# Performance work log

Measured on AMD Instinct MI355X. Metric: run time of the kernel, lower is better.

Reference implementation:

```python
import jax, jax.numpy as jnp
import numpy as np

B, L, D = 8, 2048, 512


def setup_inputs() -> dict:
    key = jax.random.key(0)
    ks = jax.random.split(key, 6)
    s = 0.02
    return {
        "q": jax.random.normal(ks[0], (B, L, D), jnp.float32),
        "k": jax.random.normal(ks[1], (B, L, D), jnp.float32),
        "v": jax.random.normal(ks[2], (B, L, D), jnp.float32),
        "Wq": jax.random.normal(ks[3], (D, D), jnp.float32) * s,
        "bq": jnp.zeros((D,), jnp.float32),
        "Wk": jax.random.normal(ks[4], (D, D), jnp.float32) * s,
        "bk": jnp.zeros((D,), jnp.float32),
        "Wv": jax.random.normal(ks[5], (D, D), jnp.float32) * s,
        "bv": jnp.zeros((D,), jnp.float32),
    }


def reference(q, k, v, Wq, bq, Wk, bk, Wv, bv):
    # Linear projections (torch Linear: x @ W.T + b)
    qp = jnp.einsum("bld,ed->ble", q, Wq) + bq
    kp = jnp.einsum("bld,ed->ble", k, Wk) + bk
    vp = jnp.einsum("bld,ed->ble", v, Wv) + bv
    # attn[b, i, j] = qp[b, i] . kp[b, j]   (no 1/sqrt(d) scaling in source)
    attn = jnp.einsum("bqd,bkd->bqk", qp, kp)
    # Faithful to torch.nn.Softmax(dim=1): normalize over the QUERY axis.
    attn = jax.nn.softmax(attn, axis=1)
    out = jnp.einsum("bqk,bkd->bqd", attn, vp)
    return out
```

## Files before the change

### kernel.cpp

```cpp
#include <hip/hip_runtime.h>
#include <math.h>


#define TKK 32

typedef __attribute__((ext_vector_type(8))) short bf16x8;
typedef __attribute__((ext_vector_type(4))) float floatx4;

typedef __attribute__((address_space(3))) short lds_short;
typedef const __attribute__((address_space(1))) short glob_short;

__device__ __forceinline__ short f2bf(float x) {
    unsigned u = __float_as_uint(x);
    u += 0x7fff + ((u >> 16) & 1);
    return (short)(u >> 16);
}
__device__ __forceinline__ float bf2f(short s) {
    return __uint_as_float(((unsigned)(unsigned short)s) << 16);
}
__device__ __forceinline__ float exp2_fast(float x) {
    float r;
    asm("v_exp_f32 %0, %1" : "=v"(r) : "v"(x));
    return r;
}

#define STAGE_SC(lane) ((((lane) & 3) ^ (((lane) >> 3) & 3)) * 8)
#define FRAG_FC(lane) (((((lane) >> 4) ^ (((lane) >> 1) & 3))) * 8)

__global__ __launch_bounds__(256) void prep(
    const float* __restrict__ q, const float* __restrict__ k,
    const float* __restrict__ v,
    const float* __restrict__ Wq, const float* __restrict__ Wk,
    const float* __restrict__ Wv,
    short* __restrict__ q_bf, short* __restrict__ k_bf, short* __restrict__ v_bf,
    short* __restrict__ Wq_bf, short* __restrict__ Wk_bf, short* __restrict__ Wv_bf,
    float* __restrict__ colsum)
{
    const int b = blockIdx.x;
    const float* in = nullptr;
    short* out = nullptr;
    long long i;
    if (b < 12288) {
        const int z = b >> 12;
        in  = (z == 0) ? q    : (z == 1) ? k    : v;
        out = (z == 0) ? q_bf : (z == 1) ? k_bf : v_bf;
        i = ((long long)(b & 4095) * 256 + threadIdx.x) * 8;
    } else if (b < 12672) {
        const int z = (b - 12288) >> 7;
        in  = (z == 0) ? Wq    : (z == 1) ? Wk    : Wv;
        out = (z == 0) ? Wq_bf : (z == 1) ? Wk_bf : Wv_bf;
        i = ((long long)((b - 12288) & 127) * 256 + threadIdx.x) * 8;
    } else {
        colsum[(b - 12672) * 256 + threadIdx.x] = 0.f;
        return;
    }
    float4 x = *(const float4*)(in + i);
    float4 y = *(const float4*)(in + i + 4);
    bf16x8 r;
    r[0] = f2bf(x.x); r[1] = f2bf(x.y); r[2] = f2bf(x.z); r[3] = f2bf(x.w);
    r[4] = f2bf(y.x); r[5] = f2bf(y.y); r[6] = f2bf(y.z); r[7] = f2bf(y.w);
    *(bf16x8*)(out + i) = r;
}

template<int TMp, int TNp, int WM, int WN, int HAS_BIAS, int OUT_BF16>
__device__ __forceinline__ void gemm_body(
    const short* __restrict__ A, const short* __restrict__ B,
    const float* __restrict__ bias, void* __restrict__ C,
    int N, int K, int m0, int n0, float escale)
{
    __shared__ short As[TMp * TKK];
    __shared__ short Bs[TNp * TKK];
    constexpr int MI = TMp / (16 * WM);
    constexpr int NJ = TNp / (16 * WN);
    constexpr int NWAVES = WM * WN;
    const int t    = threadIdx.x;
    const int wave = t >> 6;
    const int lane = t & 63;
    const int wm = (wave / WN) * (TMp / WM);
    const int wn = (wave % WN) * (TNp / WN);
    const int sr = lane >> 2;
    const int sc = STAGE_SC(lane);
    const int fc = FRAG_FC(lane);

    floatx4 acc[MI][NJ];
    #pragma unroll
    for (int i = 0; i < MI; ++i)
        #pragma unroll
        for (int j = 0; j < NJ; ++j)
            acc[i][j] = (floatx4){0.f, 0.f, 0.f, 0.f};

    for (int k0 = 0; k0 < K; k0 += TKK) {
        #pragma unroll
        for (int c = wave; c < TMp / 16; c += NWAVES)
            __builtin_amdgcn_global_load_lds(
                (glob_short*)(A + (long long)(m0 + c * 16 + sr) * K + k0 + sc),
                (lds_short*)(As + c * 512), 16, 0, 0);
        #pragma unroll
        for (int c = wave; c < TNp / 16; c += NWAVES)
            __builtin_amdgcn_global_load_lds(
                (glob_short*)(B + (long long)(n0 + c * 16 + sr) * K + k0 + sc),
                (lds_short*)(Bs + c * 512), 16, 0, 0);
        __syncthreads();
        bf16x8 af[MI], bfr[NJ];
        #pragma unroll
        for (int i = 0; i < MI; ++i)
            af[i] = *(const bf16x8*)&As[(wm + i * 16 + (lane & 15)) * TKK + fc];
        #pragma unroll
        for (int j = 0; j < NJ; ++j)
            bfr[j] = *(const bf16x8*)&Bs[(wn + j * 16 + (lane & 15)) * TKK + fc];
        #pragma unroll
        for (int i = 0; i < MI; ++i)
            #pragma unroll
            for (int j = 0; j < NJ; ++j)
                acc[i][j] = __builtin_amdgcn_mfma_f32_16x16x32_bf16(af[i], bfr[j], acc[i][j], 0, 0, 0);
        __syncthreads();
    }

    #pragma unroll
    for (int i = 0; i < MI; ++i) {
        const int rbase = m0 + wm + i * 16 + (lane >> 4) * 4;
        #pragma unroll
        for (int j = 0; j < NJ; ++j) {
            const int col = n0 + wn + j * 16 + (lane & 15);
            const float bb = HAS_BIAS ? bias[col] : 0.f;
            #pragma unroll
            for (int r = 0; r < 4; ++r) {
                const long long off = (long long)(rbase + r) * N + col;
                const float vvv = (acc[i][j][r] + bb) * escale;
                if (OUT_BF16) ((short*)C)[off] = f2bf(vvv);
                else          ((float*)C)[off] = vvv;
            }
        }
    }
}

__global__ __launch_bounds__(512) void proj_gemm(
    const short* __restrict__ x0, const short* __restrict__ x1, const short* __restrict__ x2,
    const short* __restrict__ w0, const short* __restrict__ w1, const short* __restrict__ w2,
    const float* __restrict__ b0, const float* __restrict__ b1, const float* __restrict__ b2,
    short* __restrict__ y0, short* __restrict__ y1, short* __restrict__ y2,
    int N, int K)
{
    const int z = blockIdx.z;
    const short* A    = (z == 0) ? x0 : (z == 1) ? x1 : x2;
    const short* B    = (z == 0) ? w0 : (z == 1) ? w1 : w2;
    const float* bias = (z == 0) ? b0 : (z == 1) ? b1 : b2;
    short*       C    = (z == 0) ? y0 : (z == 1) ? y1 : y2;
    const float esc   = (z == 0) ? 1.4426950408889634f : 1.0f;
    gemm_body<128, 128, 4, 2, 1, 1>(A, B, bias, C, N, K,
                                    blockIdx.x * 128, blockIdx.y * 128, esc);
}

__global__ __launch_bounds__(512) void pv_gemm(
    const short* __restrict__ Eg, const short* __restrict__ vpTg,
    float* __restrict__ outg, int N, int K,
    long long sA, long long sB, long long sC)
{
    __shared__ short As[2][128 * TKK];
    __shared__ short Bs[2][64 * TKK];
    const int bz = blockIdx.z;
    const short* A = Eg   + (long long)bz * sA;
    const short* B = vpTg + (long long)bz * sB;
    float*       C = outg + (long long)bz * sC;

    const int m0 = blockIdx.x * 128;
    const int n0 = blockIdx.y * 64;
    const int t    = threadIdx.x;
    const int wave = t >> 6;
    const int lane = t & 63;
    const int wm = (wave >> 1) * 32;
    const int wn = (wave & 1)  * 32;
    const int sr = lane >> 2;
    const int sc = STAGE_SC(lane);
    const int fc = FRAG_FC(lane);

    floatx4 acc[2][2];
    #pragma unroll
    for (int i = 0; i < 2; ++i)
        #pragma unroll
        for (int j = 0; j < 2; ++j)
            acc[i][j] = (floatx4){0.f, 0.f, 0.f, 0.f};

    for (int k0 = 0; k0 < K; k0 += 2 * TKK) {
        #pragma unroll
        for (int h = 0; h < 2; ++h) {
            const int kk = k0 + h * TKK;
            __builtin_amdgcn_global_load_lds(
                (glob_short*)(A + (long long)(m0 + wave * 16 + sr) * K + kk + sc),
                (lds_short*)(As[h] + wave * 512), 16, 0, 0);
            if (wave < 4)
                __builtin_amdgcn_global_load_lds(
                    (glob_short*)(B + (long long)(n0 + wave * 16 + sr) * K + kk + sc),
                    (lds_short*)(Bs[h] + wave * 512), 16, 0, 0);
        }
        __syncthreads();
        #pragma unroll
        for (int h = 0; h < 2; ++h) {
            bf16x8 af[2], bfr[2];
            #pragma unroll
            for (int i = 0; i < 2; ++i)
                af[i] = *(const bf16x8*)&As[h][(wm + i * 16 + (lane & 15)) * TKK + fc];
            #pragma unroll
            for (int j = 0; j < 2; ++j)
                bfr[j] = *(const bf16x8*)&Bs[h][(wn + j * 16 + (lane & 15)) * TKK + fc];
            #pragma unroll
            for (int i = 0; i < 2; ++i)
                #pragma unroll
                for (int j = 0; j < 2; ++j)
                    acc[i][j] = __builtin_amdgcn_mfma_f32_16x16x32_bf16(af[i], bfr[j], acc[i][j], 0, 0, 0);
        }
        __syncthreads();
    }

    #pragma unroll
    for (int i = 0; i < 2; ++i) {
        const int rbase = m0 + wm + i * 16 + (lane >> 4) * 4;
        #pragma unroll
        for (int j = 0; j < 2; ++j) {
            const int col = n0 + wn + j * 16 + (lane & 15);
            #pragma unroll
            for (int r = 0; r < 4; ++r)
                C[(long long)(rbase + r) * N + col] = acc[i][j][r];
        }
    }
}

__global__ __launch_bounds__(512) void gemm_nt_exp_colsum(
    const short* __restrict__ A, const short* __restrict__ B,
    short* __restrict__ E, float* __restrict__ colsum,
    int N, int K, long long sA, long long sB, long long sE)
{
    __shared__ short As[2][128 * TKK];
    __shared__ short Bs[2][128 * TKK];
    __shared__ float wsum[8][64];
    const int bz = blockIdx.z;
    A += (long long)bz * sA;
    B += (long long)bz * sB;
    E += (long long)bz * sE;
    colsum += (long long)bz * N;

    const int m0 = blockIdx.x * 128;
    const int n0 = blockIdx.y * 128;
    const int t    = threadIdx.x;
    const int wave = t >> 6;
    const int lane = t & 63;
    const int wm = (wave >> 1) * 32;
    const int wn = (wave & 1)  * 64;
    const int sr = lane >> 2;
    const int sc = STAGE_SC(lane);
    const int fc = FRAG_FC(lane);

    floatx4 acc[2][4];
    #pragma unroll
    for (int i = 0; i < 2; ++i)
        #pragma unroll
        for (int j = 0; j < 4; ++j)
            acc[i][j] = (floatx4){0.f, 0.f, 0.f, 0.f};

    for (int k0 = 0; k0 < K; k0 += 2 * TKK) {
        #pragma unroll
        for (int h = 0; h < 2; ++h) {
            const int kk = k0 + h * TKK;
            const int r = wave * 16 + sr;
            __builtin_amdgcn_global_load_lds(
                (glob_short*)(A + (long long)(m0 + r) * K + kk + sc),
                (lds_short*)(As[h] + wave * 512), 16, 0, 0);
            __builtin_amdgcn_global_load_lds(
                (glob_short*)(B + (long long)(n0 + r) * K + kk + sc),
                (lds_short*)(Bs[h] + wave * 512), 16, 0, 0);
        }
        __syncthreads();
        #pragma unroll
        for (int h = 0; h < 2; ++h) {
            bf16x8 af[2], bfr[4];
            #pragma unroll
            for (int i = 0; i < 2; ++i)
                af[i] = *(const bf16x8*)&As[h][(wm + i * 16 + (lane & 15)) * TKK + fc];
            #pragma unroll
            for (int j = 0; j < 4; ++j)
                bfr[j] = *(const bf16x8*)&Bs[h][(wn + j * 16 + (lane & 15)) * TKK + fc];
            #pragma unroll
            for (int i = 0; i < 2; ++i)
                #pragma unroll
                for (int j = 0; j < 4; ++j)
                    acc[i][j] = __builtin_amdgcn_mfma_f32_16x16x32_bf16(af[i], bfr[j], acc[i][j], 0, 0, 0);
        }
        __syncthreads();
    }

    float csum[4] = {0.f, 0.f, 0.f, 0.f};
    #pragma unroll
    for (int i = 0; i < 2; ++i) {
        const int rbase = wm + i * 16 + (lane >> 4) * 4;
        #pragma unroll
        for (int j = 0; j < 4; ++j) {
            const int col = wn + j * 16 + (lane & 15);
            #pragma unroll
            for (int r = 0; r < 4; ++r) {
                const float e = exp2_fast(acc[i][j][r]);
                E[(long long)(m0 + rbase + r) * N + (n0 + col)] = f2bf(e);
                csum[j] += e;
            }
        }
    }
    #pragma unroll
    for (int j = 0; j < 4; ++j) {
        csum[j] += __shfl_xor(csum[j], 16);
        csum[j] += __shfl_xor(csum[j], 32);
    }
    if (lane < 16) {
        #pragma unroll
        for (int j = 0; j < 4; ++j)
            wsum[wave][j * 16 + lane] = csum[j];
    }
    __syncthreads();
    if (t < 128) {
        const int half = t >> 6;
        const int col  = t & 63;
        const float s = wsum[half][col] + wsum[half + 2][col]
                      + wsum[half + 4][col] + wsum[half + 6][col];
        atomicAdd(&colsum[n0 + half * 64 + col], s);
    }
}

__global__ __launch_bounds__(256) void transpose_scale_bf16(
    const short* __restrict__ in, const float* __restrict__ colsum,
    short* __restrict__ out, int R, int Cc)
{
    __shared__ short tile[32][33];
    const int b = blockIdx.z;
    in  += (long long)b * R * Cc;
    out += (long long)b * R * Cc;
    colsum += (long long)b * R;
    const int c0 = blockIdx.x * 32, r0 = blockIdx.y * 32;
    const int tx = threadIdx.x & 31, ty = threadIdx.x >> 5;
    #pragma unroll
    for (int rr = ty; rr < 32; rr += 8) {
        const float rs = 1.f / colsum[r0 + rr];
        tile[rr][tx] = f2bf(bf2f(in[(long long)(r0 + rr) * Cc + c0 + tx]) * rs);
    }
    __syncthreads();
    #pragma unroll
    for (int rr = ty; rr < 32; rr += 8)
        out[(long long)(c0 + rr) * R + r0 + tx] = tile[tx][rr];
}

extern "C" void kernel_launch(void* const* d_in, const int* in_sizes, int n_in,
                              void* d_out, int out_size, void* d_ws, size_t ws_size,
                              hipStream_t stream) {
    const float* q  = (const float*)d_in[0];
    const float* k  = (const float*)d_in[1];
    const float* v  = (const float*)d_in[2];
    const float* Wq = (const float*)d_in[3];
    const float* bq = (const float*)d_in[4];
    const float* Wk = (const float*)d_in[5];
    const float* bk = (const float*)d_in[6];
    const float* Wv = (const float*)d_in[7];
    const float* bv = (const float*)d_in[8];
    float* out = (float*)d_out;

    const int Bb = 8, L = 2048, D = 512;
    const long long BLD = (long long)Bb * L * D;
    const long long BLL = (long long)Bb * L * L;
    const long long DD  = (long long)D * D;

    short* base  = (short*)d_ws;
    short* q_bf  = base;
    short* k_bf  = q_bf  + BLD;
    short* v_bf  = k_bf  + BLD;
    short* qp_bf = v_bf  + BLD;
    short* kp_bf = qp_bf + BLD;
    short* vp_bf = kp_bf + BLD;
    short* vpT   = vp_bf + BLD;
    short* Wq_bf = vpT   + BLD;
    short* Wk_bf = Wq_bf + DD;
    short* Wv_bf = Wk_bf + DD;
    short* E_bf  = Wv_bf + DD;
    float* colsum = (float*)(E_bf + BLL);

    dim3 blk(256);

    prep<<<dim3(12736), blk, 0, stream>>>(q, k, v, Wq, Wk, Wv,
                                          q_bf, k_bf, v_bf,
                                          Wq_bf, Wk_bf, Wv_bf, colsum);

    dim3 gproj((Bb * L) / 128, D / 128, 3);
    proj_gemm<<<gproj, dim3(512), 0, stream>>>(q_bf, k_bf, v_bf,
                                               Wq_bf, Wk_bf, Wv_bf,
                                               bq, bk, bv,
                                               qp_bf, kp_bf, vp_bf, D, D);

    dim3 gS(L / 128, L / 128, Bb);
    gemm_nt_exp_colsum<<<gS, dim3(512), 0, stream>>>(qp_bf, kp_bf, E_bf, colsum,
                                                     L, D,
                                                     (long long)L * D, (long long)L * D,
                                                     (long long)L * L);

    dim3 gT(D / 32, L / 32, Bb);
    transpose_scale_bf16<<<gT, blk, 0, stream>>>(vp_bf, colsum, vpT, L, D);

    dim3 gO(L / 128, D / 64, Bb);
    pv_gemm<<<gO, dim3(512), 0, stream>>>(E_bf, vpT, out, D, L,
                                          (long long)L * L, (long long)D * L,
                                          (long long)L * D);
}
```

Baseline: 301.6 us.

## Fuse fp32-to-bf16 conversion of q/k/v into projection GEMM loads

```diff
diff --git a/kernel.cpp b/kernel.cpp
--- a/kernel.cpp
+++ b/kernel.cpp
@@ -9,6 +9,8 @@
 
 typedef __attribute__((address_space(3))) short lds_short;
 typedef const __attribute__((address_space(1))) short glob_short;
+typedef __attribute__((address_space(3))) float lds_float;
+typedef const __attribute__((address_space(1))) float glob_float;
 
 __device__ __forceinline__ short f2bf(float x) {
     unsigned u = __float_as_uint(x);
@@ -28,127 +30,111 @@
 #define FRAG_FC(lane) (((((lane) >> 4) ^ (((lane) >> 1) & 3))) * 8)
 
 __global__ __launch_bounds__(256) void prep(
-    const float* __restrict__ q, const float* __restrict__ k,
-    const float* __restrict__ v,
     const float* __restrict__ Wq, const float* __restrict__ Wk,
     const float* __restrict__ Wv,
-    short* __restrict__ q_bf, short* __restrict__ k_bf, short* __restrict__ v_bf,
     short* __restrict__ Wq_bf, short* __restrict__ Wk_bf, short* __restrict__ Wv_bf,
     float* __restrict__ colsum)
 {
     const int b = blockIdx.x;
-    const float* in = nullptr;
-    short* out = nullptr;
-    long long i;
-    if (b < 12288) {
-        const int z = b >> 12;
-        in  = (z == 0) ? q    : (z == 1) ? k    : v;
-        out = (z == 0) ? q_bf : (z == 1) ? k_bf : v_bf;
-        i = ((long long)(b & 4095) * 256 + threadIdx.x) * 8;
-    } else if (b < 12672) {
-        const int z = (b - 12288) >> 7;
-        in  = (z == 0) ? Wq    : (z == 1) ? Wk    : Wv;
-        out = (z == 0) ? Wq_bf : (z == 1) ? Wk_bf : Wv_bf;
-        i = ((long long)((b - 12288) & 127) * 256 + threadIdx.x) * 8;
+    if (b < 384) {
+        const int z = b >> 7;
+        const float* in = (z == 0) ? Wq : (z == 1) ? Wk : Wv;
+        short* out = (z == 0) ? Wq_bf : (z == 1) ? Wk_bf : Wv_bf;
+        const long long i = ((long long)(b & 127) * 256 + threadIdx.x) * 8;
+        float4 x = *(const float4*)(in + i);
+        float4 y = *(const float4*)(in + i + 4);
+        bf16x8 r;
+        r[0] = f2bf(x.x); r[1] = f2bf(x.y); r[2] = f2bf(x.z); r[3] = f2bf(x.w);
+        r[4] = f2bf(y.x); r[5] = f2bf(y.y); r[6] = f2bf(y.z); r[7] = f2bf(y.w);
+        *(bf16x8*)(out + i) = r;
     } else {
-        colsum[(b - 12672) * 256 + threadIdx.x] = 0.f;
-        return;
-    }
-    float4 x = *(const float4*)(in + i);
-    float4 y = *(const float4*)(in + i + 4);
-    bf16x8 r;
-    r[0] = f2bf(x.x); r[1] = f2bf(x.y); r[2] = f2bf(x.z); r[3] = f2bf(x.w);
-    r[4] = f2bf(y.x); r[5] = f2bf(y.y); r[6] = f2bf(y.z); r[7] = f2bf(y.w);
-    *(bf16x8*)(out + i) = r;
-}
-
-template<int TMp, int TNp, int WM, int WN, int HAS_BIAS, int OUT_BF16>
-__device__ __forceinline__ void gemm_body(
-    const short* __restrict__ A, const short* __restrict__ B,
-    const float* __restrict__ bias, void* __restrict__ C,
-    int N, int K, int m0, int n0, float escale)
-{
-    __shared__ short As[TMp * TKK];
-    __shared__ short Bs[TNp * TKK];
-    constexpr int MI = TMp / (16 * WM);
-    constexpr int NJ = TNp / (16 * WN);
-    constexpr int NWAVES = WM * WN;
-    const int t    = threadIdx.x;
-    const int wave = t >> 6;
-    const int lane = t & 63;
-    const int wm = (wave / WN) * (TMp / WM);
-    const int wn = (wave % WN) * (TNp / WN);
-    const int sr = lane >> 2;
-    const int sc = STAGE_SC(lane);
-    const int fc = FRAG_FC(lane);
-
-    floatx4 acc[MI][NJ];
-    #pragma unroll
-    for (int i = 0; i < MI; ++i)
-        #pragma unroll
-        for (int j = 0; j < NJ; ++j)
-            acc[i][j] = (floatx4){0.f, 0.f, 0.f, 0.f};
-
-    for (int k0 = 0; k0 < K; k0 += TKK) {
-        #pragma unroll
-        for (int c = wave; c < TMp / 16; c += NWAVES)
-            __builtin_amdgcn_global_load_lds(
-                (glob_short*)(A + (long long)(m0 + c * 16 + sr) * K + k0 + sc),
-                (lds_short*)(As + c * 512), 16, 0, 0);
-        #pragma unroll
-        for (int c = wave; c < TNp / 16; c += NWAVES)
-            __builtin_amdgcn_global_load_lds(
-                (glob_short*)(B + (long long)(n0 + c * 16 + sr) * K + k0 + sc),
-                (lds_short*)(Bs + c * 512), 16, 0, 0);
-        __syncthreads();
-        bf16x8 af[MI], bfr[NJ];
-        #pragma unroll
-        for (int i = 0; i < MI; ++i)
-            af[i] = *(const bf16x8*)&As[(wm + i * 16 + (lane & 15)) * TKK + fc];
-        #pragma unroll
-        for (int j = 0; j < NJ; ++j)
-            bfr[j] = *(const bf16x8*)&Bs[(wn + j * 16 + (lane & 15)) * TKK + fc];
-        #pragma unroll
-        for (int i = 0; i < MI; ++i)
-            #pragma unroll
-            for (int j = 0; j < NJ; ++j)
-                acc[i][j] = __builtin_amdgcn_mfma_f32_16x16x32_bf16(af[i], bfr[j], acc[i][j], 0, 0, 0);
-        __syncthreads();
-    }
-
-    #pragma unroll
-    for (int i = 0; i < MI; ++i) {
-        const int rbase = m0 + wm + i * 16 + (lane >> 4) * 4;
-        #pragma unroll
-        for (int j = 0; j < NJ; ++j) {
-            const int col = n0 + wn + j * 16 + (lane & 15);
-            const float bb = HAS_BIAS ? bias[col] : 0.f;
-            #pragma unroll
-            for (int r = 0; r < 4; ++r) {
-                const long long off = (long long)(rbase + r) * N + col;
-                const float vvv = (acc[i][j][r] + bb) * escale;
-                if (OUT_BF16) ((short*)C)[off] = f2bf(vvv);
-                else          ((float*)C)[off] = vvv;
-            }
-        }
+        colsum[(b - 384) * 256 + threadIdx.x] = 0.f;
     }
 }
 
 __global__ __launch_bounds__(512) void proj_gemm(
-    const short* __restrict__ x0, const short* __restrict__ x1, const short* __restrict__ x2,
+    const float* __restrict__ x0, const float* __restrict__ x1, const float* __restrict__ x2,
     const short* __restrict__ w0, const short* __restrict__ w1, const short* __restrict__ w2,
     const float* __restrict__ b0, const float* __restrict__ b1, const float* __restrict__ b2,
     short* __restrict__ y0, short* __restrict__ y1, short* __restrict__ y2,
     int N, int K)
 {
     const int z = blockIdx.z;
-    const short* A    = (z == 0) ? x0 : (z == 1) ? x1 : x2;
+    const float* A    = (z == 0) ? x0 : (z == 1) ? x1 : x2;
     const short* B    = (z == 0) ? w0 : (z == 1) ? w1 : w2;
     const float* bias = (z == 0) ? b0 : (z == 1) ? b1 : b2;
     short*       C    = (z == 0) ? y0 : (z == 1) ? y1 : y2;
     const float esc   = (z == 0) ? 1.4426950408889634f : 1.0f;
-    gemm_body<128, 128, 4, 2, 1, 1>(A, B, bias, C, N, K,
-                                    blockIdx.x * 128, blockIdx.y * 128, esc);
+
+    __shared__ float Asf[128 * TKK];
+    __shared__ short Bs[128 * TKK];
+    const int t    = threadIdx.x;
+    const int wave = t >> 6;
+    const int lane = t & 63;
+    const int wm = (wave >> 1) * 32;
+    const int wn = (wave & 1)  * 64;
+    const int sr = lane >> 2;
+    const int sc = STAGE_SC(lane);
+    const int fc = FRAG_FC(lane);
+    const int m0 = blockIdx.x * 128;
+    const int n0 = blockIdx.y * 128;
+    const int ar8 = lane >> 3;
+    const int au  = ((lane & 7) ^ ar8) * 4;
+    const int h   = lane >> 4;
+
+    floatx4 acc[2][4];
+    #pragma unroll
+    for (int i = 0; i < 2; ++i)
+        #pragma unroll
+        for (int j = 0; j < 4; ++j)
+            acc[i][j] = (floatx4){0.f, 0.f, 0.f, 0.f};
+
+    for (int k0 = 0; k0 < K; k0 += TKK) {
+        #pragma unroll
+        for (int cc = 0; cc < 2; ++cc) {
+            const int c = wave * 2 + cc;
+            __builtin_amdgcn_global_load_lds(
+                (glob_float*)(A + (long long)(m0 + c * 8 + ar8) * K + k0 + au),
+                (lds_float*)(Asf + c * 256), 16, 0, 0);
+        }
+        __builtin_amdgcn_global_load_lds(
+            (glob_short*)(B + (long long)(n0 + wave * 16 + sr) * K + k0 + sc),
+            (lds_short*)(Bs + wave * 512), 16, 0, 0);
+        __syncthreads();
+        bf16x8 af[2], bfr[4];
+        #pragma unroll
+        for (int i = 0; i < 2; ++i) {
+            const int R = wm + i * 16 + (lane & 15);
+            const float4 u0 = *(const float4*)&Asf[R * TKK + (((h * 2)     ^ (R & 7)) * 4)];
+            const float4 u1 = *(const float4*)&Asf[R * TKK + (((h * 2 + 1) ^ (R & 7)) * 4)];
+            af[i][0] = f2bf(u0.x); af[i][1] = f2bf(u0.y);
+            af[i][2] = f2bf(u0.z); af[i][3] = f2bf(u0.w);
+            af[i][4] = f2bf(u1.x); af[i][5] = f2bf(u1.y);
+            af[i][6] = f2bf(u1.z); af[i][7] = f2bf(u1.w);
+        }
+        #pragma unroll
+        for (int j = 0; j < 4; ++j)
+            bfr[j] = *(const bf16x8*)&Bs[(wn + j * 16 + (lane & 15)) * TKK + fc];
+        #pragma unroll
+        for (int i = 0; i < 2; ++i)
+            #pragma unroll
+            for (int j = 0; j < 4; ++j)
+                acc[i][j] = __builtin_amdgcn_mfma_f32_16x16x32_bf16(af[i], bfr[j], acc[i][j], 0, 0, 0);
+        __syncthreads();
+    }
+
+    #pragma unroll
+    for (int i = 0; i < 2; ++i) {
+        const int rbase = m0 + wm + i * 16 + (lane >> 4) * 4;
+        #pragma unroll
+        for (int j = 0; j < 4; ++j) {
+            const int col = n0 + wn + j * 16 + (lane & 15);
+            const float bb = bias[col];
+            #pragma unroll
+            for (int r = 0; r < 4; ++r)
+                C[(long long)(rbase + r) * N + col] = f2bf((acc[i][j][r] + bb) * esc);
+        }
+    }
 }
 
 __global__ __launch_bounds__(512) void pv_gemm(
@@ -365,10 +351,7 @@
     const long long DD  = (long long)D * D;
 
     short* base  = (short*)d_ws;
-    short* q_bf  = base;
-    short* k_bf  = q_bf  + BLD;
-    short* v_bf  = k_bf  + BLD;
-    short* qp_bf = v_bf  + BLD;
+    short* qp_bf = base;
     short* kp_bf = qp_bf + BLD;
     short* vp_bf = kp_bf + BLD;
     short* vpT   = vp_bf + BLD;
@@ -380,12 +363,10 @@
 
     dim3 blk(256);
 
-    prep<<<dim3(12736), blk, 0, stream>>>(q, k, v, Wq, Wk, Wv,
-                                          q_bf, k_bf, v_bf,
-                                          Wq_bf, Wk_bf, Wv_bf, colsum);
+    prep<<<dim3(448), blk, 0, stream>>>(Wq, Wk, Wv, Wq_bf, Wk_bf, Wv_bf, colsum);
 
     dim3 gproj((Bb * L) / 128, D / 128, 3);
-    proj_gemm<<<gproj, dim3(512), 0, stream>>>(q_bf, k_bf, v_bf,
+    proj_gemm<<<gproj, dim3(512), 0, stream>>>(q, k, v,
                                                Wq_bf, Wk_bf, Wv_bf,
                                                bq, bk, bv,
                                                qp_bf, kp_bf, vp_bf, D, D);
```

After: 300.3 us. About the same (-0.4%).
